# Optimization experiments

Measured on AMD Instinct MI355X. Metric: run time of the kernel, lower is better.

Reference implementation:

```python
import jax, jax.numpy as jnp
import numpy as np
from jax import lax

RADIUS = 2  # scipy grey_opening size=2 -> 2x2 flat structuring element


def _window_filter(x, size, pad_lo, pad_hi, is_min):
    """Sliding min/max over the last two (spatial) dims of [B,C,H,W].
    Boundary handling matches scipy mode='reflect' (== numpy 'symmetric')."""
    xp = jnp.pad(x, ((0, 0), (0, 0), (pad_lo, pad_hi), (pad_lo, pad_hi)), mode='symmetric')
    init = jnp.array(np.inf if is_min else -np.inf, dtype=x.dtype)
    op = lax.min if is_min else lax.max
    return lax.reduce_window(xp, init, op,
                             window_dimensions=(1, 1, size, size),
                             window_strides=(1, 1, 1, 1),
                             padding='VALID')


def grey_opening(x, size):
    # scipy grey_erosion offsets per axis: [-(size//2), ..., size-1-size//2]
    lo, hi = size // 2, size - 1 - size // 2
    eroded = _window_filter(x, size, lo, hi, is_min=True)
    # grey_dilation uses the reflected structuring element -> offsets [-hi, ..., lo]
    opened = _window_filter(eroded, size, hi, lo, is_min=False)
    return opened


def setup_inputs() -> dict:
    key = jax.random.key(0)
    labels = jax.random.uniform(key, (16, 8, 512, 512), dtype=jnp.float32)
    return {"labels": labels}


def reference(labels):
    opened = grey_opening(labels, RADIUS)
    # MSE between labels and their (detached) grey opening
    return jnp.mean(jnp.square(labels - opened))
```

## Files before the change

### kernel.cpp

```cpp
#include <hip/hip_runtime.h>

#define IMG_H 512
#define IMG_W 512
#define NIMG 128
#define CHUNK 32
#define NCHUNK (IMG_H / CHUNK)
#define THREADS 256
#define WPB (THREADS / 64)
#define NBLOCKS (NIMG * NCHUNK / WPB)

__global__ __launch_bounds__(THREADS)
void opening_mse_kernel(const float* __restrict__ X, float* __restrict__ out) {
    const int lane = threadIdx.x & 63;
    const int gw   = blockIdx.x * WPB + (threadIdx.x >> 6);
    const int n     = gw >> 4;
    const int chunk = gw & (NCHUNK - 1);
    const int s = chunk * CHUNK;
    const int e = s + CHUNK;
    const float* __restrict__ img = X + (size_t)n * (IMG_H * IMG_W);
    const int cb = lane << 3;
    const int rmax = (e < IMG_H) ? e : (IMG_H - 1);

    auto ld = [&](int r, float4& a, float4& b) {
        const float* __restrict__ p = img + (size_t)r * IMG_W + cb;
        a = *reinterpret_cast<const float4*>(p);
        b = *reinterpret_cast<const float4*>(p + 4);
    };

    auto mkh = [&](const float4& a, const float4& b, float (&h)[9]) {
        float xl = __shfl_up(b.w, 1, 64);
        if (lane == 0) xl = a.x;
        float xr = __shfl_down(a.x, 1, 64);
        h[0] = fminf(xl, a.x);
        h[1] = fminf(a.x, a.y);
        h[2] = fminf(a.y, a.z);
        h[3] = fminf(a.z, a.w);
        h[4] = fminf(a.w, b.x);
        h[5] = fminf(b.x, b.y);
        h[6] = fminf(b.y, b.z);
        h[7] = fminf(b.z, b.w);
        h[8] = (lane == 63) ? h[7] : fminf(b.w, xr);
    };

    float hprev[9], hd[8];
    float4 xa, xb;

    {
        float4 ta, tb;
        ld(s > 0 ? s - 1 : 0, ta, tb);
        mkh(ta, tb, hprev);
        ld(s, xa, xb);
        float hcur[9], E[9];
        mkh(xa, xb, hcur);
        #pragma unroll
        for (int k = 0; k < 9; ++k) E[k] = fminf(hprev[k], hcur[k]);
        #pragma unroll
        for (int k = 0; k < 8; ++k) hd[k] = fmaxf(E[k], E[k + 1]);
        #pragma unroll
        for (int k = 0; k < 9; ++k) hprev[k] = hcur[k];
    }

    float4 q1a0, q1b0, q1a1, q1b1;
    float4 q2a0, q2b0, q2a1, q2b1;
    ld(s + 1, q1a0, q1b0);
    ld(s + 2, q1a1, q1b1);
    ld(s + 3, q2a0, q2b0);
    ld(s + 4, q2a1, q2b1);

    float acc = 0.0f;
    #pragma unroll 2
    for (int t = 0; t < CHUNK / 2; ++t) {
        const int a0 = s + 1 + 2 * t;
        const int a1 = a0 + 1;

        float4 c0a = q1a0, c0b = q1b0, c1a = q1a1, c1b = q1b1;
        q1a0 = q2a0; q1b0 = q2b0; q1a1 = q2a1; q1b1 = q2b1;
        int r0 = a0 + 4; r0 = r0 < rmax ? r0 : rmax;
        int r1 = a0 + 5; r1 = r1 < rmax ? r1 : rmax;
        ld(r0, q2a0, q2b0);
        ld(r1, q2a1, q2b1);

        float h0[9], hd0[8];
        {
            float E[9];
            mkh(c0a, c0b, h0);
            #pragma unroll
            for (int k = 0; k < 9; ++k) E[k] = fminf(hprev[k], h0[k]);
            #pragma unroll
            for (int k = 0; k < 8; ++k) hd0[k] = fmaxf(E[k], E[k + 1]);
        }
        {
            float d;
            d = xa.x - fmaxf(hd[0], hd0[0]); acc = fmaf(d, d, acc);
            d = xa.y - fmaxf(hd[1], hd0[1]); acc = fmaf(d, d, acc);
            d = xa.z - fmaxf(hd[2], hd0[2]); acc = fmaf(d, d, acc);
            d = xa.w - fmaxf(hd[3], hd0[3]); acc = fmaf(d, d, acc);
            d = xb.x - fmaxf(hd[4], hd0[4]); acc = fmaf(d, d, acc);
            d = xb.y - fmaxf(hd[5], hd0[5]); acc = fmaf(d, d, acc);
            d = xb.z - fmaxf(hd[6], hd0[6]); acc = fmaf(d, d, acc);
            d = xb.w - fmaxf(hd[7], hd0[7]); acc = fmaf(d, d, acc);
        }

        float h1[9], hd1[8];
        if (a1 < IMG_H) {
            float E[9];
            mkh(c1a, c1b, h1);
            #pragma unroll
            for (int k = 0; k < 9; ++k) E[k] = fminf(h0[k], h1[k]);
            #pragma unroll
            for (int k = 0; k < 8; ++k) hd1[k] = fmaxf(E[k], E[k + 1]);
            #pragma unroll
            for (int k = 0; k < 9; ++k) hprev[k] = h1[k];
        } else {
            #pragma unroll
            for (int k = 0; k < 8; ++k) hd1[k] = hd0[k];
        }
        {
            float d;
            d = c0a.x - fmaxf(hd0[0], hd1[0]); acc = fmaf(d, d, acc);
            d = c0a.y - fmaxf(hd0[1], hd1[1]); acc = fmaf(d, d, acc);
            d = c0a.z - fmaxf(hd0[2], hd1[2]); acc = fmaf(d, d, acc);
            d = c0a.w - fmaxf(hd0[3], hd1[3]); acc = fmaf(d, d, acc);
            d = c0b.x - fmaxf(hd0[4], hd1[4]); acc = fmaf(d, d, acc);
            d = c0b.y - fmaxf(hd0[5], hd1[5]); acc = fmaf(d, d, acc);
            d = c0b.z - fmaxf(hd0[6], hd1[6]); acc = fmaf(d, d, acc);
            d = c0b.w - fmaxf(hd0[7], hd1[7]); acc = fmaf(d, d, acc);
        }

        #pragma unroll
        for (int k = 0; k < 8; ++k) hd[k] = hd1[k];
        xa = c1a; xb = c1b;
    }

    #pragma unroll
    for (int off = 32; off > 0; off >>= 1)
        acc += __shfl_down(acc, off, 64);

    __shared__ float wsum[WPB];
    const int wid = threadIdx.x >> 6;
    if (lane == 0) wsum[wid] = acc;
    __syncthreads();
    if (threadIdx.x == 0) {
        float sblk = wsum[0] + wsum[1] + wsum[2] + wsum[3];
        atomicAdd(out, sblk * (1.0f / 33554432.0f));
    }
}

extern "C" void kernel_launch(void* const* d_in, const int* in_sizes, int n_in,
                              void* d_out, int out_size, void* d_ws, size_t ws_size,
                              hipStream_t stream) {
    const float* X = (const float*)d_in[0];
    float* out = (float*)d_out;
    hipMemsetAsync(out, 0, sizeof(float), stream);
    opening_mse_kernel<<<NBLOCKS, THREADS, 0, stream>>>(X, out);
}
```

Measured before the change: 33.80 us.

## Split image rows across two waves per chunk with deeper row prefetch

Each wave now covers half the image width (256 columns, one float4 per lane) instead of the full row (two float4 per lane), so twice as many waves run. Each lane loads one extra edge scalar per row so the halo across the split is handled. The software prefetch depth grows from two row pairs to four. The aim is more parallelism and more memory requests in flight to hide load latency on a bandwidth-bound stencil. The cost is redundant edge loads, extra scalar loads per row and more waves.

```diff
diff --git a/kernel.cpp b/kernel.cpp
--- a/kernel.cpp
+++ b/kernel.cpp
@@ -5,67 +5,74 @@
 #define NIMG 128
 #define CHUNK 32
 #define NCHUNK (IMG_H / CHUNK)
+#define HALVES 2
 #define THREADS 256
 #define WPB (THREADS / 64)
-#define NBLOCKS (NIMG * NCHUNK / WPB)
+#define NWAVES (NIMG * NCHUNK * HALVES)
+#define NBLOCKS (NWAVES / WPB)
 
 __global__ __launch_bounds__(THREADS)
 void opening_mse_kernel(const float* __restrict__ X, float* __restrict__ out) {
     const int lane = threadIdx.x & 63;
     const int gw   = blockIdx.x * WPB + (threadIdx.x >> 6);
-    const int n     = gw >> 4;
-    const int chunk = gw & (NCHUNK - 1);
+    const int n     = gw >> 5;
+    const int chunk = (gw >> 1) & (NCHUNK - 1);
+    const int half  = gw & 1;
     const int s = chunk * CHUNK;
     const int e = s + CHUNK;
+    const int wbase = half << 8;
     const float* __restrict__ img = X + (size_t)n * (IMG_H * IMG_W);
-    const int cb = lane << 3;
+    const int c0 = wbase + (lane << 2);
+    const int cl = (wbase > 0) ? wbase - 1 : 0;
+    const int cr = (wbase + 256 < IMG_W) ? wbase + 256 : IMG_W - 1;
+    const bool rightEdge = (wbase + 256 >= IMG_W);
+    const int ec = (lane == 0) ? cl : cr;
     const int rmax = (e < IMG_H) ? e : (IMG_H - 1);
 
-    auto ld = [&](int r, float4& a, float4& b) {
-        const float* __restrict__ p = img + (size_t)r * IMG_W + cb;
-        a = *reinterpret_cast<const float4*>(p);
-        b = *reinterpret_cast<const float4*>(p + 4);
+    auto ld = [&](int r, float4& a, float& edge) {
+        const float* __restrict__ row = img + (size_t)r * IMG_W;
+        a = *reinterpret_cast<const float4*>(row + c0);
+        edge = row[ec];
     };
 
-    auto mkh = [&](const float4& a, const float4& b, float (&h)[9]) {
-        float xl = __shfl_up(b.w, 1, 64);
-        if (lane == 0) xl = a.x;
+    auto mkh = [&](const float4& a, float edge, float (&h)[5]) {
+        float xl = __shfl_up(a.w, 1, 64);
+        if (lane == 0) xl = edge;
         float xr = __shfl_down(a.x, 1, 64);
+        if (lane == 63) xr = edge;
         h[0] = fminf(xl, a.x);
         h[1] = fminf(a.x, a.y);
         h[2] = fminf(a.y, a.z);
         h[3] = fminf(a.z, a.w);
-        h[4] = fminf(a.w, b.x);
-        h[5] = fminf(b.x, b.y);
-        h[6] = fminf(b.y, b.z);
-        h[7] = fminf(b.z, b.w);
-        h[8] = (lane == 63) ? h[7] : fminf(b.w, xr);
+        h[4] = fminf(a.w, xr);
+        if (rightEdge && lane == 63) h[4] = h[3];
     };
 
-    float hprev[9], hd[8];
-    float4 xa, xb;
+    float hprev[5], hd[4];
+    float4 xa;
 
     {
-        float4 ta, tb;
-        ld(s > 0 ? s - 1 : 0, ta, tb);
-        mkh(ta, tb, hprev);
-        ld(s, xa, xb);
-        float hcur[9], E[9];
-        mkh(xa, xb, hcur);
+        float4 ta; float te;
+        ld(s > 0 ? s - 1 : 0, ta, te);
+        mkh(ta, te, hprev);
+        float xe;
+        ld(s, xa, xe);
+        float hcur[5], E[5];
+        mkh(xa, xe, hcur);
         #pragma unroll
-        for (int k = 0; k < 9; ++k) E[k] = fminf(hprev[k], hcur[k]);
+        for (int k = 0; k < 5; ++k) E[k] = fminf(hprev[k], hcur[k]);
         #pragma unroll
-        for (int k = 0; k < 8; ++k) hd[k] = fmaxf(E[k], E[k + 1]);
+        for (int k = 0; k < 4; ++k) hd[k] = fmaxf(E[k], E[k + 1]);
         #pragma unroll
-        for (int k = 0; k < 9; ++k) hprev[k] = hcur[k];
+        for (int k = 0; k < 5; ++k) hprev[k] = hcur[k];
     }
 
-    float4 q1a0, q1b0, q1a1, q1b1;
-    float4 q2a0, q2b0, q2a1, q2b1;
-    ld(s + 1, q1a0, q1b0);
-    ld(s + 2, q1a1, q1b1);
-    ld(s + 3, q2a0, q2b0);
-    ld(s + 4, q2a1, q2b1);
+    float4 A10, A11, A20, A21, A30, A31, A40, A41;
+    float  E10, E11, E20, E21, E30, E31, E40, E41;
+    ld(s + 1, A10, E10);  ld(s + 2, A11, E11);
+    ld(s + 3, A20, E20);  ld(s + 4, A21, E21);
+    ld(s + 5, A30, E30);  ld(s + 6, A31, E31);
+    ld(s + 7, A40, E40);  ld(s + 8, A41, E41);
 
     float acc = 0.0f;
     #pragma unroll 2
@@ -73,21 +80,24 @@
         const int a0 = s + 1 + 2 * t;
         const int a1 = a0 + 1;
 
-        float4 c0a = q1a0, c0b = q1b0, c1a = q1a1, c1b = q1b1;
-        q1a0 = q2a0; q1b0 = q2b0; q1a1 = q2a1; q1b1 = q2b1;
-        int r0 = a0 + 4; r0 = r0 < rmax ? r0 : rmax;
-        int r1 = a0 + 5; r1 = r1 < rmax ? r1 : rmax;
-        ld(r0, q2a0, q2b0);
-        ld(r1, q2a1, q2b1);
+        float4 c0a = A10; float c0e = E10;
+        float4 c1a = A11; float c1e = E11;
+        A10 = A20; E10 = E20;  A11 = A21; E11 = E21;
+        A20 = A30; E20 = E30;  A21 = A31; E21 = E31;
+        A30 = A40; E30 = E40;  A31 = A41; E31 = E41;
+        int r0 = a0 + 8; r0 = r0 < rmax ? r0 : rmax;
+        int r1 = a0 + 9; r1 = r1 < rmax ? r1 : rmax;
+        ld(r0, A40, E40);
+        ld(r1, A41, E41);
 
-        float h0[9], hd0[8];
+        float h0[5], hd0[4];
         {
-            float E[9];
-            mkh(c0a, c0b, h0);
+            float E[5];
+            mkh(c0a, c0e, h0);
             #pragma unroll
-            for (int k = 0; k < 9; ++k) E[k] = fminf(hprev[k], h0[k]);
+            for (int k = 0; k < 5; ++k) E[k] = fminf(hprev[k], h0[k]);
             #pragma unroll
-            for (int k = 0; k < 8; ++k) hd0[k] = fmaxf(E[k], E[k + 1]);
+            for (int k = 0; k < 4; ++k) hd0[k] = fmaxf(E[k], E[k + 1]);
         }
         {
             float d;
@@ -95,25 +105,21 @@
             d = xa.y - fmaxf(hd[1], hd0[1]); acc = fmaf(d, d, acc);
             d = xa.z - fmaxf(hd[2], hd0[2]); acc = fmaf(d, d, acc);
             d = xa.w - fmaxf(hd[3], hd0[3]); acc = fmaf(d, d, acc);
-            d = xb.x - fmaxf(hd[4], hd0[4]); acc = fmaf(d, d, acc);
-            d = xb.y - fmaxf(hd[5], hd0[5]); acc = fmaf(d, d, acc);
-            d = xb.z - fmaxf(hd[6], hd0[6]); acc = fmaf(d, d, acc);
-            d = xb.w - fmaxf(hd[7], hd0[7]); acc = fmaf(d, d, acc);
         }
 
-        float h1[9], hd1[8];
+        float hd1[4];
         if (a1 < IMG_H) {
-            float E[9];
-            mkh(c1a, c1b, h1);
+            float h1[5], E[5];
+            mkh(c1a, c1e, h1);
             #pragma unroll
-            for (int k = 0; k < 9; ++k) E[k] = fminf(h0[k], h1[k]);
+            for (int k = 0; k < 5; ++k) E[k] = fminf(h0[k], h1[k]);
             #pragma unroll
-            for (int k = 0; k < 8; ++k) hd1[k] = fmaxf(E[k], E[k + 1]);
+            for (int k = 0; k < 4; ++k) hd1[k] = fmaxf(E[k], E[k + 1]);
             #pragma unroll
-            for (int k = 0; k < 9; ++k) hprev[k] = h1[k];
+            for (int k = 0; k < 5; ++k) hprev[k] = h1[k];
         } else {
             #pragma unroll
-            for (int k = 0; k < 8; ++k) hd1[k] = hd0[k];
+            for (int k = 0; k < 4; ++k) hd1[k] = hd0[k];
         }
         {
             float d;
@@ -121,15 +127,11 @@
             d = c0a.y - fmaxf(hd0[1], hd1[1]); acc = fmaf(d, d, acc);
             d = c0a.z - fmaxf(hd0[2], hd1[2]); acc = fmaf(d, d, acc);
             d = c0a.w - fmaxf(hd0[3], hd1[3]); acc = fmaf(d, d, acc);
-            d = c0b.x - fmaxf(hd0[4], hd1[4]); acc = fmaf(d, d, acc);
-            d = c0b.y - fmaxf(hd0[5], hd1[5]); acc = fmaf(d, d, acc);
-            d = c0b.z - fmaxf(hd0[6], hd1[6]); acc = fmaf(d, d, acc);
-            d = c0b.w - fmaxf(hd0[7], hd1[7]); acc = fmaf(d, d, acc);
         }
 
         #pragma unroll
-        for (int k = 0; k < 8; ++k) hd[k] = hd1[k];
-        xa = c1a; xb = c1b;
+        for (int k = 0; k < 4; ++k) hd[k] = hd1[k];
+        xa = c1a;
     }
 
     #pragma unroll
```

After: 38.29 us. 13.3% more time.
